# Kernel optimization log

Measured on AMD Instinct MI355X. Metric: run time of the kernel, lower is better.

## Reference

```python
import jax, jax.numpy as jnp
import numpy as np

B, T, D, H = 2, 2048, 1024, 16
NEG = -65504.0


def setup_inputs() -> dict:
    key = jax.random.key(0)
    ks = jax.random.split(key, 12)
    std = float(np.sqrt(2.0 / (D + D)))  # xavier_normal for square weights
    inp = {
        'q': jax.random.normal(ks[0], (B, T, D), jnp.float32),
        'k': jax.random.normal(ks[1], (B, T, D), jnp.float32),
        'v': jax.random.normal(ks[2], (B, T, D), jnp.float32),
        'mask': jax.random.randint(ks[3], (B, T), 0, 2, jnp.int32),
        # weights stored as (in, out) so y = x @ W + b
        'Wq': jax.random.normal(ks[4], (D, D), jnp.float32) * std,
        'bq': jnp.zeros((D,), jnp.float32),
        'Wk': jax.random.normal(ks[5], (D, D), jnp.float32) * std,
        'bk': jnp.zeros((D,), jnp.float32),
        'Wv': jax.random.normal(ks[6], (D, D), jnp.float32) * std,
        'bv': jnp.zeros((D,), jnp.float32),
        'Wo': jax.random.normal(ks[7], (D, D), jnp.float32) * std,
        'bo': jnp.zeros((D,), jnp.float32),
    }
    return inp


def reference(q, k, v, mask, Wq, bq, Wk, bk, Wv, bv, Wo, bo):
    b, t, _ = q.shape
    dim_a = Wq.shape[1]
    dh = dim_a // H
    # projections, then split into heads: (b, t, H, dh)
    qh = (q @ Wq + bq).reshape(b, t, H, dh)
    kh = (k @ Wk + bk).reshape(b, t, H, dh)
    vh = (v @ Wv + bv).reshape(b, t, H, dh)
    # NOTE: module scales by 1/sqrt(dim_a) with the FULL dim_a, not per-head
    a = jnp.einsum('bthd,bshd->bhts', qh, kh) / jnp.sqrt(jnp.float32(dim_a))
    # 2D mask broadcasts over query positions: (b, 1, 1, t_keys)
    a = jnp.where(mask[:, None, None, :] == 0, NEG, a)
    a = jax.nn.softmax(a, axis=-1)  # dropout_prob=0 (eval mode)
    o = jnp.einsum('bhts,bshd->bthd', a, vh).reshape(b, t, dim_a)
    return o @ Wo + bo
```

## Files before the change

### kernel.cpp

```cpp
#include <hip/hip_runtime.h>
#include <hip/hip_bf16.h>
#include <math.h>

#define B_ 2
#define T_ 2048
#define D_ 1024
#define H_ 16
#define QSCALE (0.03125f * 1.44269504088896f)

typedef _Float16 f16;
using f16x4 = __attribute__((ext_vector_type(4))) _Float16;
using f16x8 = __attribute__((ext_vector_type(8))) _Float16;
using f32x4 = __attribute__((ext_vector_type(4))) float;

__device__ __forceinline__ void gl16(const void* g, void* l) {
  __builtin_amdgcn_global_load_lds(
      (__attribute__((address_space(1))) void*)g,
      (__attribute__((address_space(3))) void*)l, 16, 0, 0);
}

__global__ __launch_bounds__(256) void prep(
    const float* __restrict__ q, const float* __restrict__ k,
    const float* __restrict__ v, const int* __restrict__ mask,
    const float* __restrict__ Wq, const float* __restrict__ Wk,
    const float* __restrict__ Wv, const float* __restrict__ Wo,
    const float* __restrict__ bq, const float* __restrict__ bk,
    const float* __restrict__ bv, const float* __restrict__ bo,
    f16* __restrict__ xqkv, f16* __restrict__ Wt, float* __restrict__ bias,
    int* __restrict__ idx, int* __restrict__ inv, int* __restrict__ nk,
    f16* __restrict__ khc) {
  __shared__ float sh[64][65];
  const int bid = blockIdx.x;
  const int tid = threadIdx.x;

  if (bid < 6144) {
    const int z = bid / 2048;
    const float* src = (z == 0) ? q : (z == 1) ? k : v;
    const size_t i = ((size_t)(bid % 2048) * 256 + tid) * 8;
    float4 a = *(const float4*)(src + i);
    float4 b = *(const float4*)(src + i + 4);
    f16x8 o;
    o[0] = (f16)a.x; o[1] = (f16)a.y; o[2] = (f16)a.z; o[3] = (f16)a.w;
    o[4] = (f16)b.x; o[5] = (f16)b.y; o[6] = (f16)b.z; o[7] = (f16)b.w;
    *(f16x8*)(xqkv + (size_t)z * 4194304 + i) = o;
  } else if (bid < 7168) {
    const int id = bid - 6144;
    const int z = id >> 8;
    const int k0 = ((id >> 4) & 15) * 64, n0 = (id & 15) * 64;
    const float* W = (z == 0) ? Wq : (z == 1) ? Wk : (z == 2) ? Wv : Wo;
    const int r = tid >> 2, c0 = (tid & 3) * 16;
#pragma unroll
    for (int i = 0; i < 4; ++i)
      *(float4*)&sh[r][c0 + 4 * i] =
          *(const float4*)&W[(size_t)(k0 + r) * 1024 + n0 + c0 + 4 * i];
    __syncthreads();
    f16 tmp[16];
#pragma unroll
    for (int i = 0; i < 16; ++i) tmp[i] = (f16)sh[c0 + i][r];
    f16* dst = Wt + (size_t)z * 1048576 + (size_t)(n0 + r) * 1024 + k0 + c0;
    *(f16x8*)dst = *(f16x8*)&tmp[0];
    *(f16x8*)(dst + 8) = *(f16x8*)&tmp[8];
  } else if (bid < 7184) {
    const int i = (bid - 7168) * 256 + tid;
    const int z = i >> 10;
    const float* s = (z == 0) ? bq : (z == 1) ? bk : (z == 2) ? bv : bo;
    bias[i] = s[i & 1023];
  } else {
    const int b = bid - 7184;
    int* cnt = (int*)sh;
    int loc[8];
    int c = 0;
#pragma unroll
    for (int i = 0; i < 8; ++i) {
      loc[i] = mask[b * T_ + tid * 8 + i];
      c += loc[i];
    }
    cnt[tid] = c;
    __syncthreads();
    for (int off = 1; off < 256; off <<= 1) {
      int vsh = (tid >= off) ? cnt[tid - off] : 0;
      __syncthreads();
      cnt[tid] += vsh;
      __syncthreads();
    }
    int pos = cnt[tid] - c;
#pragma unroll
    for (int i = 0; i < 8; ++i) {
      const int t = tid * 8 + i;
      if (loc[i]) {
        idx[b * T_ + pos] = t;
        inv[b * T_ + t] = pos;
        ++pos;
      } else {
        inv[b * T_ + t] = -1;
      }
    }
    const int n = cnt[255];
    if (tid == 255) nk[b] = n;
    const int nkt = (n + 63) >> 6;
    const int npadrows = (nkt << 6) - n;
    uint4 z4 = {0u, 0u, 0u, 0u};
    f16* base = khc + ((size_t)b * T_ + n) * D_;
    for (int i = tid; i < npadrows * 128; i += 256)
      *(uint4*)(base + (size_t)i * 8) = z4;
  }
}

template <int TM, typename OT>
__global__ __launch_bounds__(256) void gemm_bt(
    const f16* __restrict__ Xb, const f16* __restrict__ Wtb,
    const float* __restrict__ biasb, void* __restrict__ C0,
    void* __restrict__ C1, void* __restrict__ C2,
    const int* __restrict__ inv, int M, int N, int K, float qscale) {
  constexpr int FM = TM / 32;
  __shared__ __align__(16) f16 As[TM * 32];
  __shared__ __align__(16) f16 Bs[128 * 32];
  const int z = blockIdx.z;
  const f16* X  = Xb  + (size_t)z * M * K;
  const f16* Wt = Wtb + (size_t)z * N * K;
  const float* bias = biasb + (size_t)z * N;
  OT* C = (OT*)((z == 0) ? C0 : (z == 1) ? C1 : C2);
  const float scl = (z == 0) ? qscale : 1.f;

  const int tid = threadIdx.x;
  const int wave = tid >> 6, lane = tid & 63;
  const int quad = lane >> 4, l16 = lane & 15;
  const int wm = wave & 1, wn = wave >> 1;
  const int m0 = blockIdx.y * TM, n0 = blockIdx.x * 128;

  f32x4 acc[FM][4] = {};

  const f16* asrc = X  + (size_t)(m0 + (tid >> 2)) * K + (tid & 3) * 8;
  const f16* bsrc = Wt + (size_t)(n0 + (tid >> 2)) * K + (tid & 3) * 8;
  char* aldst = (char*)As + tid * 16;
  char* bldst = (char*)Bs + tid * 16;
  const size_t rstep = (size_t)64 * K;

  const int NK = K >> 5;
  for (int kt = 0; kt < NK; ++kt) {
    if (kt) __syncthreads();
    gl16(asrc, aldst);
    if constexpr (TM == 128) gl16(asrc + rstep, aldst + 4096);
    gl16(bsrc, bldst);
    gl16(bsrc + rstep, bldst + 4096);
    asrc += 32; bsrc += 32;
    __syncthreads();

    f16x8 af[FM], bf[4];
#pragma unroll
    for (int t = 0; t < FM; ++t)
      af[t] = *(const f16x8*)&As[((TM / 2) * wm + 16 * t + l16) * 32 + quad * 8];
#pragma unroll
    for (int t = 0; t < 4; ++t)
      bf[t] = *(const f16x8*)&Bs[(64 * wn + 16 * t + l16) * 32 + quad * 8];
#pragma unroll
    for (int i = 0; i < FM; ++i)
#pragma unroll
      for (int j = 0; j < 4; ++j)
        acc[i][j] = __builtin_amdgcn_mfma_f32_16x16x32_f16(af[i], bf[j], acc[i][j], 0, 0, 0);
  }

  const int cm = m0 + (TM / 2) * wm + 4 * quad;
  const int cn = n0 + 64 * wn + l16;
  float bv[4];
#pragma unroll
  for (int tn = 0; tn < 4; ++tn) bv[tn] = bias[cn + 16 * tn];

  if (inv != nullptr && z == 1) {
    const int bb = m0 >> 11;
#pragma unroll
    for (int tm = 0; tm < FM; ++tm) {
#pragma unroll
      for (int r = 0; r < 4; ++r) {
        const int m = cm + 16 * tm + r;
        const int j = inv[m];
        if (j >= 0) {
          OT* row = C + ((size_t)(bb << 11) + j) * N;
#pragma unroll
          for (int tn = 0; tn < 4; ++tn)
            row[cn + 16 * tn] = (OT)(acc[tm][tn][r] + bv[tn]);
        }
      }
    }
  } else {
#pragma unroll
    for (int tm = 0; tm < FM; ++tm)
#pragma unroll
      for (int r = 0; r < 4; ++r) {
        OT* row = C + (size_t)(cm + 16 * tm + r) * N;
#pragma unroll
        for (int tn = 0; tn < 4; ++tn)
          row[cn + 16 * tn] = (OT)((acc[tm][tn][r] + bv[tn]) * scl);
      }
  }
}

__global__ __launch_bounds__(256) void vtrans(
    const f16* __restrict__ vh, const int* __restrict__ idx,
    const int* __restrict__ nk, f16* __restrict__ vhT) {
  const int tt = blockIdx.x, bh = blockIdx.y;
  const int b = bh >> 4, h = bh & 15;
  const int n = nk[b];
  const int nkt = (n + 63) >> 6;
  if (tt >= nkt) return;
  __shared__ f16 t[64][72];
  const int tid = threadIdx.x;
  const int r = tid >> 2, cq = 16 * (tid & 3);

  const int j = tt * 64 + r;
  uint4 v0 = {0u, 0u, 0u, 0u}, v1 = {0u, 0u, 0u, 0u};
  if (j < n) {
    const int tsrc = idx[b * T_ + j];
    const uint4* src = (const uint4*)(vh + ((size_t)b * T_ + tsrc) * D_ + h * 64 + cq);
    v0 = src[0]; v1 = src[1];
  }
  *(uint4*)&t[r][cq]     = v0;
  *(uint4*)&t[r][cq + 8] = v1;
  __syncthreads();

  f16 tmp[16];
#pragma unroll
  for (int xx = 0; xx < 16; ++xx) {
    int x = (xx + r) & 15;
    tmp[x] = t[cq + x][r];
  }
  f16* dst = vhT + ((size_t)bh * 64 + r) * T_ + tt * 64 + cq;
  *(uint4*)&dst[0] = *(uint4*)&tmp[0];
  *(uint4*)&dst[8] = *(uint4*)&tmp[8];
}

__global__ __launch_bounds__(512) void attn_mfma(
    const f16* __restrict__ qh, const f16* __restrict__ khc,
    const f16* __restrict__ vhT, const int* __restrict__ nkd,
    f16* __restrict__ oat) {
  __shared__ f16 Ks[64][72];
  __shared__ f16 Vt[64][72];
  __shared__ f16 Ps[8][16][72];

  const int qt = blockIdx.x, bh = blockIdx.y;
  const int b = bh >> 4, h = bh & 15;
  const int tid = threadIdx.x;
  const int wave = tid >> 6, lane = tid & 63;
  const int quad = lane >> 4, l16 = lane & 15;
  const int sr = tid >> 3, sq = 8 * (tid & 7);

  const int n = nkd[b];
  const int nkt = (n + 63) >> 6;
  const int npad = (nkt << 6) - n;

  f16x8 qf[2];
  {
    const f16* qp = qh + ((size_t)(b * T_ + qt * 128 + wave * 16 + l16)) * D_ + h * 64 + quad * 8;
    qf[0] = *(const f16x8*)qp;
    qf[1] = *(const f16x8*)(qp + 32);
  }

  float lsum = 0.f;
  f32x4 o[4] = {};

  const f16* kbase = khc + (size_t)b * T_ * D_ + h * 64;
  const f16* vbase = vhT + ((size_t)bh * 64 + sr) * T_;

  uint4 kr, vr;
  auto load_kv = [&](int kt) {
    kr = *(const uint4*)(kbase + (size_t)(kt * 64 + sr) * D_ + sq);
    vr = *(const uint4*)(vbase + kt * 64 + sq);
  };
  if (nkt > 0) load_kv(0);

  for (int kt = 0; kt < nkt; ++kt) {
    *(uint4*)&Ks[sr][sq] = kr;
    *(uint4*)&Vt[sr][sq] = vr;
    __syncthreads();
    if (kt + 1 < nkt) load_kv(kt + 1);

#pragma unroll
    for (int tn = 0; tn < 4; ++tn) {
      f16x8 kf0 = *(const f16x8*)&Ks[16 * tn + l16][quad * 8];
      f16x8 kf1 = *(const f16x8*)&Ks[16 * tn + l16][32 + quad * 8];
      f32x4 s = {0.f, 0.f, 0.f, 0.f};
      s = __builtin_amdgcn_mfma_f32_16x16x32_f16(kf0, qf[0], s, 0, 0, 0);
      s = __builtin_amdgcn_mfma_f32_16x16x32_f16(kf1, qf[1], s, 0, 0, 0);
      float p0 = exp2f(s[0]), p1 = exp2f(s[1]);
      float p2 = exp2f(s[2]), p3 = exp2f(s[3]);
      lsum += (p0 + p1) + (p2 + p3);
      f16x4 pk;
      pk[0] = (f16)p0; pk[1] = (f16)p1; pk[2] = (f16)p2; pk[3] = (f16)p3;
      *(f16x4*)&Ps[wave][l16][16 * tn + 4 * quad] = pk;
    }

    f16x8 pf0 = *(const f16x8*)&Ps[wave][l16][quad * 8];
    f16x8 pf1 = *(const f16x8*)&Ps[wave][l16][32 + quad * 8];
#pragma unroll
    for (int t = 0; t < 4; ++t) {
      f16x8 vf0 = *(const f16x8*)&Vt[16 * t + l16][quad * 8];
      f16x8 vf1 = *(const f16x8*)&Vt[16 * t + l16][32 + quad * 8];
      o[t] = __builtin_amdgcn_mfma_f32_16x16x32_f16(pf0, vf0, o[t], 0, 0, 0);
      o[t] = __builtin_amdgcn_mfma_f32_16x16x32_f16(pf1, vf1, o[t], 0, 0, 0);
    }
    __syncthreads();
  }

  {
    float ls = lsum;
    ls += __shfl_xor(ls, 16);
    ls += __shfl_xor(ls, 32);
    ls -= (float)npad;
    const size_t orow = (size_t)(b * T_ + qt * 128 + wave * 16 + 4 * quad);
#pragma unroll
    for (int r = 0; r < 4; ++r) {
      const float iv = 1.f / __shfl(ls, 4 * quad + r);
#pragma unroll
      for (int t = 0; t < 4; ++t)
        oat[(orow + r) * D_ + h * 64 + 16 * t + l16] = (f16)(o[t][r] * iv);
    }
  }
}

extern "C" void kernel_launch(void* const* d_in, const int* in_sizes, int n_in,
                              void* d_out, int out_size, void* d_ws, size_t ws_size,
                              hipStream_t stream) {
  const float* q  = (const float*)d_in[0];
  const float* k  = (const float*)d_in[1];
  const float* v  = (const float*)d_in[2];
  const int* mask = (const int*)d_in[3];
  const float* Wq = (const float*)d_in[4];
  const float* bq = (const float*)d_in[5];
  const float* Wk = (const float*)d_in[6];
  const float* bk = (const float*)d_in[7];
  const float* Wv = (const float*)d_in[8];
  const float* bv = (const float*)d_in[9];
  const float* Wo = (const float*)d_in[10];
  const float* bo = (const float*)d_in[11];
  float* out = (float*)d_out;

  char* ws = (char*)d_ws;
  f16* xqkv  = (f16*)(ws);
  f16* Wt    = (f16*)(ws + 25165824);
  f16* qh    = (f16*)(ws + 33554432);
  f16* vh    = (f16*)(ws + 41943040);
  f16* khc   = (f16*)(ws + 50331648);
  float* bsw = (float*)(ws + 58720256);
  int* idx   = (int*)(ws + 58736640);
  int* inv   = (int*)(ws + 58753024);
  int* nk    = (int*)(ws + 58769408);
  f16* vhT   = (f16*)(ws);
  f16* oat   = (f16*)(ws + 8388608);

  const int M = B_ * T_;
  dim3 blk(256);

  prep<<<dim3(7186), blk, 0, stream>>>(q, k, v, mask, Wq, Wk, Wv, Wo,
                                       bq, bk, bv, bo, xqkv, Wt, bsw,
                                       idx, inv, nk, khc);

  gemm_bt<128, f16><<<dim3(8, 32, 3), blk, 0, stream>>>(
      xqkv, Wt, bsw, qh, khc, vh, inv, M, D_, D_, QSCALE);

  vtrans<<<dim3(32, 32), blk, 0, stream>>>(vh, idx, nk, vhT);

  attn_mfma<<<dim3(16, 32), dim3(512), 0, stream>>>(qh, khc, vhT, nk, oat);

  gemm_bt<64, float><<<dim3(8, 64, 1), blk, 0, stream>>>(
      oat, Wt + 3145728, bsw + 3072, out, out, out, nullptr, M, D_, D_, 1.f);
}
```

Measured before the change: 230.7 us.

## Replace QKV projection GEMM with 256x256-tile, 4-stage async LDS pipelined kernel

Adds a new gemm8 kernel for the fused Q/K/V projection. It uses 512-thread blocks with 256x256 output tiles and a 4-deep ring of LDS buffers filled by global_load_lds, with explicit vmcnt waits and swizzled LDS reads. It also uses the 16x16x32 f16 MFMA and raises wave priority around the MFMA block. The goal is higher data reuse per block and better overlap of loads with compute than the 128x128 gemm_bt. The cost is only 192 blocks, which may underfill the GPU, plus heavy register pressure from the 8x4 accumulator tile and a 128KB LDS footprint per block.

```diff
diff --git a/kernel.cpp b/kernel.cpp
--- a/kernel.cpp
+++ b/kernel.cpp
@@ -106,6 +106,120 @@
   }
 }
 
+__global__ __launch_bounds__(512, 2) void gemm8(
+    const f16* __restrict__ Xb, const f16* __restrict__ Wtb,
+    const float* __restrict__ biasb, void* __restrict__ C0,
+    void* __restrict__ C1, void* __restrict__ C2,
+    const int* __restrict__ inv, float qscale) {
+  __shared__ __align__(16) char lds[131072];
+  const int z = blockIdx.z;
+  const f16* X  = Xb  + (size_t)z * (4096 * 1024);
+  const f16* Wt = Wtb + (size_t)z * (1024 * 1024);
+  const float* bias = biasb + (size_t)z * 1024;
+  f16* C = (f16*)((z == 0) ? C0 : (z == 1) ? C1 : C2);
+  const float scl = (z == 0) ? qscale : 1.f;
+
+  const int tid = threadIdx.x;
+  const int wave = tid >> 6, lane = tid & 63;
+  const int quad = lane >> 4, l16 = lane & 15;
+  const int wm = wave & 1, wn = wave >> 1;
+  const int m0 = blockIdx.y * 256, n0 = blockIdx.x * 256;
+
+  const int r0 = tid >> 2;
+  const int ssw = (tid & 3) ^ ((r0 >> 1) & 3);
+  const f16* ap0 = X  + (size_t)(m0 + r0) * 1024 + ssw * 8;
+  const f16* ap1 = ap0 + (size_t)128 * 1024;
+  const f16* bp0 = Wt + (size_t)(n0 + r0) * 1024 + ssw * 8;
+  const f16* bp1 = bp0 + (size_t)128 * 1024;
+  char* al = lds + tid * 16;
+  char* bl = lds + 65536 + tid * 16;
+
+  const int sw16 = 16 * (quad ^ ((l16 >> 1) & 3));
+
+  f32x4 acc[8][4] = {};
+
+#define G8_ISSUE(tt) do {                                                   \
+    const int _b = (tt) & 3; const int _ko = (tt) * 32;                     \
+    gl16(ap0 + _ko, al + _b * 16384);                                       \
+    gl16(ap1 + _ko, al + _b * 16384 + 8192);                                \
+    gl16(bp0 + _ko, bl + _b * 16384);                                       \
+    gl16(bp1 + _ko, bl + _b * 16384 + 8192);                                \
+  } while (0)
+
+#define G8_WAIT(n) asm volatile("s_waitcnt vmcnt(" #n ")" ::: "memory")
+
+#define G8_COMPUTE(tt) do {                                                 \
+    __builtin_amdgcn_s_barrier();                                           \
+    const char* _Ab = lds + ((tt) & 3) * 16384;                             \
+    const char* _Bb = lds + 65536 + ((tt) & 3) * 16384;                     \
+    f16x8 af[8], bf[4];                                                     \
+    _Pragma("unroll")                                                       \
+    for (int mi = 0; mi < 8; ++mi)                                          \
+      af[mi] = *(const f16x8*)(_Ab + (128 * wm + 16 * mi + l16) * 64 + sw16); \
+    _Pragma("unroll")                                                       \
+    for (int ni = 0; ni < 4; ++ni)                                          \
+      bf[ni] = *(const f16x8*)(_Bb + (64 * wn + 16 * ni + l16) * 64 + sw16); \
+    __builtin_amdgcn_s_setprio(1);                                          \
+    _Pragma("unroll")                                                       \
+    for (int mi = 0; mi < 8; ++mi)                                          \
+      _Pragma("unroll")                                                     \
+      for (int ni = 0; ni < 4; ++ni)                                        \
+        acc[mi][ni] = __builtin_amdgcn_mfma_f32_16x16x32_f16(               \
+            af[mi], bf[ni], acc[mi][ni], 0, 0, 0);                          \
+    __builtin_amdgcn_s_setprio(0);                                          \
+    __builtin_amdgcn_s_barrier();                                           \
+  } while (0)
+
+  G8_ISSUE(0); G8_ISSUE(1); G8_ISSUE(2);
+
+  for (int tt = 0; tt < 29; ++tt) {
+    G8_ISSUE(tt + 3);
+    G8_WAIT(12);
+    G8_COMPUTE(tt);
+  }
+  G8_WAIT(8);  G8_COMPUTE(29);
+  G8_WAIT(4);  G8_COMPUTE(30);
+  G8_WAIT(0);  G8_COMPUTE(31);
+
+#undef G8_ISSUE
+#undef G8_WAIT
+#undef G8_COMPUTE
+
+  const int cm = m0 + 128 * wm + 4 * quad;
+  const int cn = n0 + 64 * wn + l16;
+  float bv[4];
+#pragma unroll
+  for (int ni = 0; ni < 4; ++ni) bv[ni] = bias[cn + 16 * ni];
+
+  if (inv != nullptr && z == 1) {
+    const int bb = m0 >> 11;
+#pragma unroll
+    for (int mi = 0; mi < 8; ++mi) {
+#pragma unroll
+      for (int r = 0; r < 4; ++r) {
+        const int m = cm + 16 * mi + r;
+        const int j = inv[m];
+        if (j >= 0) {
+          f16* row = C + ((size_t)(bb << 11) + j) * 1024;
+#pragma unroll
+          for (int ni = 0; ni < 4; ++ni)
+            row[cn + 16 * ni] = (f16)(acc[mi][ni][r] + bv[ni]);
+        }
+      }
+    }
+  } else {
+#pragma unroll
+    for (int mi = 0; mi < 8; ++mi)
+#pragma unroll
+      for (int r = 0; r < 4; ++r) {
+        f16* row = C + (size_t)(cm + 16 * mi + r) * 1024;
+#pragma unroll
+        for (int ni = 0; ni < 4; ++ni)
+          row[cn + 16 * ni] = (f16)((acc[mi][ni][r] + bv[ni]) * scl);
+      }
+  }
+}
+
 template <int TM, typename OT>
 __global__ __launch_bounds__(256) void gemm_bt(
     const f16* __restrict__ Xb, const f16* __restrict__ Wtb,
@@ -354,8 +468,8 @@
                                        bq, bk, bv, bo, xqkv, Wt, bsw,
                                        idx, inv, nk, khc);
 
-  gemm_bt<128, f16><<<dim3(8, 32, 3), blk, 0, stream>>>(
-      xqkv, Wt, bsw, qh, khc, vh, inv, M, D_, D_, QSCALE);
+  gemm8<<<dim3(4, 16, 3), dim3(512), 0, stream>>>(
+      xqkv, Wt, bsw, qh, khc, vh, inv, QSCALE);
 
   vtrans<<<dim3(32, 32), blk, 0, stream>>>(vh, idx, nk, vhT);
 
```

New measurement: 225.0 us. -2.5%, faster.
